# Kernel tuning notes

Hardware: AMD Instinct MI355X
Metric: run time of the kernel (lower is better)

## Reference

```python
import jax, jax.numpy as jnp
import numpy as np

LEAKY = 0.2
K = 8  # hard-coded topk in the torch module
NUM_HEADS = 3


def _knn_mean(x):
    # x: [B, N, C] -> mean of K nearest neighbor features (self included), [B, N, C]
    sq = jnp.sum(x * x, axis=-1)                                   # [B, N]
    d2 = sq[:, :, None] + sq[:, None, :] - 2.0 * jnp.einsum('bnc,bmc->bnm', x, x)
    _, idx = jax.lax.top_k(-d2, K)                                  # smallest distances, [B, N, K]
    neighbors = jax.vmap(lambda xb, ib: xb[ib])(x, idx)             # [B, N, K, C]
    return neighbors.mean(axis=2)


def _mlp(h, W1, b1, W2, b2):
    h = h @ W1.T + b1
    h = jnp.where(h > 0, h, LEAKY * h)                              # LeakyReLU(0.2)
    return h @ W2.T + b2


def _mha(x, Wqkv, bqkv, Wo, bo):
    # x: [S, L, C] self-attention, torch nn.MultiheadAttention semantics
    S, L, C = x.shape
    hd = C // NUM_HEADS
    qkv = x @ Wqkv.T + bqkv                                         # [S, L, 3C]
    q, k, v = jnp.split(qkv, 3, axis=-1)
    def heads(t):
        return t.reshape(S, L, NUM_HEADS, hd).transpose(0, 2, 1, 3)  # [S, H, L, hd]
    q, k, v = heads(q), heads(k), heads(v)
    scores = jnp.einsum('shld,shmd->shlm', q, k) / np.float32(np.sqrt(hd))
    att = jax.nn.softmax(scores, axis=-1)
    o = jnp.einsum('shlm,shmd->shld', att, v).transpose(0, 2, 1, 3).reshape(S, L, C)
    return o @ Wo.T + bo


def setup_inputs() -> dict:
    key = jax.random.key(0)
    ks = jax.random.split(key, 8)
    B, N, C, Hd, HOPS = 4, 4096, 96, 192, 3
    s_in = 1.0 / np.sqrt(C)
    s_hd = 1.0 / np.sqrt(Hd)
    return {
        'xyz': jax.random.normal(ks[0], (B, N, C), jnp.float32),
        'W1': jax.random.normal(ks[1], (HOPS, Hd, C), jnp.float32) * s_in,
        'b1': jnp.zeros((HOPS, Hd), jnp.float32),
        'W2': jax.random.normal(ks[2], (HOPS, C, Hd), jnp.float32) * s_hd,
        'b2': jnp.zeros((HOPS, C), jnp.float32),
        'in_proj_w': jax.random.normal(ks[3], (3 * C, C), jnp.float32) * s_in,
        'in_proj_b': jnp.zeros((3 * C,), jnp.float32),
        'out_proj_w': jax.random.normal(ks[4], (C, C), jnp.float32) * s_in,
        'out_proj_b': jnp.zeros((C,), jnp.float32),
    }


def reference(xyz, W1, b1, W2, b2, in_proj_w, in_proj_b, out_proj_w, out_proj_b):
    B, N, C = xyz.shape
    HOPS = W1.shape[0]
    hop_feats = [xyz]
    cur = xyz
    for h in range(HOPS):
        nb = _knn_mean(cur)                                         # [B, N, C]
        enc = _mlp(nb, W1[h], b1[h], W2[h], b2[h])                  # [B, N, C]
        hop_feats.append(enc)
        cur = enc
    stacked = jnp.stack(hop_feats, axis=2).reshape(B * N, HOPS + 1, C)
    att = _mha(stacked, in_proj_w, in_proj_b, out_proj_w, out_proj_b)
    return att.reshape(B, N, HOPS + 1, C).mean(axis=2)
```

## Files before the change

kernel.cpp:

```cpp
#include <hip/hip_runtime.h>
#include <cfloat>

namespace {

constexpr int Bb    = 4;
constexpr int Nn    = 4096;
constexpr int Cc    = 96;
constexpr int Ll    = 4;
constexpr int NPTS  = Bb * Nn;
constexpr int KP    = 100;
constexpr int CS    = 4;
constexpr int TK    = 10;
constexpr int NCROW = CS * 4 * TK;
constexpr int LP    = 104;
constexpr int NSEL  = 24;

typedef __attribute__((ext_vector_type(8))) short bf16x8;
typedef __attribute__((ext_vector_type(4))) float f32x4;

__device__ inline ushort f2bf(float x) {
    unsigned u = __float_as_uint(x);
    return (ushort)((u + 0x7FFF + ((u >> 16) & 1)) >> 16);
}

template<int T>
__device__ inline void lexins(float v, int vi, float (&bd)[T], int (&bi)[T]) {
    if (v < bd[T - 1] || (v == bd[T - 1] && vi < bi[T - 1])) {
        #pragma unroll
        for (int t = 0; t < T; ++t) {
            if (v < bd[t] || (v == bd[t] && vi < bi[t])) {
                float tv = bd[t]; bd[t] = v;  v  = tv;
                int   ti = bi[t]; bi[t] = vi; vi = ti;
            }
        }
    }
}

template<bool COPY>
__global__ __launch_bounds__(64) void sqcvt_kernel(const float* __restrict__ src0,
                                                   float* __restrict__ A32,
                                                   float* __restrict__ sqnp,
                                                   ushort* __restrict__ A16, int h) {
    const int p = blockIdx.x * 64 + threadIdx.x;
    const float4* xs = reinterpret_cast<const float4*>(
        COPY ? src0 + (size_t)p * Cc : src0 + (size_t)(p * Ll + h) * Cc);
    float4 x[24];
    #pragma unroll
    for (int i = 0; i < 24; ++i) x[i] = xs[i];
    if (COPY) {
        float4* d = reinterpret_cast<float4*>(A32 + (size_t)p * Ll * Cc);
        #pragma unroll
        for (int i = 0; i < 24; ++i) d[i] = x[i];
    }
    float r[8];
    r[0] = __fmul_rn(x[0].x, x[0].x); r[1] = __fmul_rn(x[0].y, x[0].y);
    r[2] = __fmul_rn(x[0].z, x[0].z); r[3] = __fmul_rn(x[0].w, x[0].w);
    r[4] = __fmul_rn(x[1].x, x[1].x); r[5] = __fmul_rn(x[1].y, x[1].y);
    r[6] = __fmul_rn(x[1].z, x[1].z); r[7] = __fmul_rn(x[1].w, x[1].w);
    #pragma unroll
    for (int g = 1; g < 12; ++g) {
        float4 va = x[2 * g], vb = x[2 * g + 1];
        r[0] = __fadd_rn(r[0], __fmul_rn(va.x, va.x));
        r[1] = __fadd_rn(r[1], __fmul_rn(va.y, va.y));
        r[2] = __fadd_rn(r[2], __fmul_rn(va.z, va.z));
        r[3] = __fadd_rn(r[3], __fmul_rn(va.w, va.w));
        r[4] = __fadd_rn(r[4], __fmul_rn(vb.x, vb.x));
        r[5] = __fadd_rn(r[5], __fmul_rn(vb.y, vb.y));
        r[6] = __fadd_rn(r[6], __fmul_rn(vb.z, vb.z));
        r[7] = __fadd_rn(r[7], __fmul_rn(vb.w, vb.w));
    }
    float L = __fadd_rn(__fadd_rn(r[0], r[1]), __fadd_rn(r[2], r[3]));
    float R = __fadd_rn(__fadd_rn(r[4], r[5]), __fadd_rn(r[6], r[7]));
    sqnp[p] = __fadd_rn(L, R);
    #pragma unroll
    for (int j = 0; j < 12; ++j) {
        float4 v0 = x[2 * j], v1 = x[2 * j + 1];
        uint4 o;
        o.x = (unsigned)f2bf(v0.x) | ((unsigned)f2bf(v0.y) << 16);
        o.y = (unsigned)f2bf(v0.z) | ((unsigned)f2bf(v0.w) << 16);
        o.z = (unsigned)f2bf(v1.x) | ((unsigned)f2bf(v1.y) << 16);
        o.w = (unsigned)f2bf(v1.z) | ((unsigned)f2bf(v1.w) << 16);
        *reinterpret_cast<uint4*>(A16 + (size_t)p * 96 + j * 8) = o;
    }
}

__global__ __launch_bounds__(256) void knn_mfma_kernel(const ushort* __restrict__ A16,
                                                       const float* __restrict__ sqnp,
                                                       unsigned* __restrict__ fkey) {
    __shared__ alignas(16) char uqk[20480];
    __shared__ ushort dbt[2][64 * LP];
    __shared__ float  sqf[2][64];
    ushort* qt   = (ushort*)uqk;
    float*  klds = (float*)uqk;

    const int q0    = blockIdx.x * 64;
    const int cs    = blockIdx.y;
    const int pbase = (q0 >> 12) << 12;
    const int col0  = cs * (Nn / CS);
    const int tid   = threadIdx.x;
    const int w     = tid >> 6;
    const int l     = tid & 63;
    constexpr int NCH = (Nn / CS) / 64;

    {
        int r = tid >> 2, q = tid & 3;
        const uint4* s = reinterpret_cast<const uint4*>(A16 + (size_t)(q0 + r) * 96 + q * 24);
        uint4* d = reinterpret_cast<uint4*>(qt + r * LP + q * 24);
        d[0] = s[0]; d[1] = s[1]; d[2] = s[2];
        const uint4* s2 = reinterpret_cast<const uint4*>(
            A16 + (size_t)(pbase + col0 + r) * 96 + q * 24);
        uint4* d2 = reinterpret_cast<uint4*>(dbt[0] + r * LP + q * 24);
        d2[0] = s2[0]; d2[1] = s2[1]; d2[2] = s2[2];
    }
    if (tid < 64) sqf[0][tid] = -0.5f * sqnp[pbase + col0 + tid];
    __syncthreads();

    const int qrow = w * 16 + (l & 15);
    const int koff = (l >> 4) * 8;
    const int lb4  = (l >> 4) * 4;
    bf16x8 bq[3];
    #pragma unroll
    for (int s = 0; s < 3; ++s)
        bq[s] = *reinterpret_cast<const bf16x8*>(qt + qrow * LP + koff + 32 * s);
    __syncthreads();

    unsigned bd[TK];
    #pragma unroll
    for (int t = 0; t < TK; ++t) bd[t] = 0x00800000u;
    float kd = -FLT_MAX;

    for (int c = 0; c < NCH; ++c) {
        const int buf = c & 1;
        if (c + 1 < NCH) {
            int r = tid >> 2, q = tid & 3;
            const uint4* s = reinterpret_cast<const uint4*>(
                A16 + (size_t)(pbase + col0 + (c + 1) * 64 + r) * 96 + q * 24);
            uint4* d = reinterpret_cast<uint4*>(dbt[buf ^ 1] + r * LP + q * 24);
            d[0] = s[0]; d[1] = s[1]; d[2] = s[2];
            if (tid < 64) sqf[buf ^ 1][tid] = -0.5f * sqnp[pbase + col0 + (c + 1) * 64 + tid];
        }

        f32x4 acc[4];
        #pragma unroll
        for (int sub = 0; sub < 4; ++sub) {
            acc[sub] = *reinterpret_cast<const f32x4*>(&sqf[buf][sub * 16 + lb4]);
            #pragma unroll
            for (int s = 0; s < 3; ++s) {
                bf16x8 a = *reinterpret_cast<const bf16x8*>(
                    dbt[buf] + (sub * 16 + (l & 15)) * LP + koff + 32 * s);
                acc[sub] = __builtin_amdgcn_mfma_f32_16x16x32_bf16(a, bq[s], acc[sub], 0, 0, 0);
            }
        }

        unsigned mask = 0;
        #pragma unroll
        for (int sub = 0; sub < 4; ++sub) {
            float m = fmaxf(fmaxf(acc[sub][0], acc[sub][1]),
                            fmaxf(acc[sub][2], acc[sub][3]));
            if (m > kd) {
                *reinterpret_cast<f32x4*>(&klds[tid * 20 + sub * 4]) = acc[sub];
                unsigned mb = (acc[sub][0] > kd ? 1u : 0u) |
                              (acc[sub][1] > kd ? 2u : 0u) |
                              (acc[sub][2] > kd ? 4u : 0u) |
                              (acc[sub][3] > kd ? 8u : 0u);
                mask |= mb << (sub * 4);
            }
        }
        while (mask) {
            int s = __builtin_ctz(mask); mask &= mask - 1;
            float v = klds[tid * 20 + s];
            if (v > kd) {
                unsigned b   = __float_as_uint(v);
                unsigned key = ((b ^ (unsigned)(((int)b >> 31) | 0x80000000)) & ~511u)
                               | (511u - (unsigned)(c * 16 + s));
                #pragma unroll
                for (int t = 0; t < TK; ++t) {
                    unsigned hi = key > bd[t] ? key : bd[t];
                    key         = key > bd[t] ? bd[t] : key;
                    bd[t] = hi;
                }
                unsigned u = bd[TK - 1] & ~511u;
                kd = __uint_as_float((u & 0x80000000u) ? (u ^ 0x80000000u) : ~u);
            }
        }
        __syncthreads();
    }

    const int qg = q0 + qrow;
    const size_t obase = (size_t)qg * NCROW + (cs * 4 + (l >> 4)) * TK;
    #pragma unroll
    for (int t = 0; t < TK; ++t) fkey[obase + t] = bd[t];
}

__device__ inline int decode_idx(unsigned key, int f) {
    int pos = 511 - (int)(key & 511u);
    int c = pos >> 4, s = pos & 15;
    return (f >> 2) * (Nn / CS) + c * 64 + ((s >> 2) << 4) + (f & 3) * 4 + (s & 3);
}

__global__ __launch_bounds__(256) void rescore_mean_kernel(const float* __restrict__ A32,
                                                           const float* __restrict__ sqnp,
                                                           const unsigned* __restrict__ fkey,
                                                           float* __restrict__ nb, int h) {
    __shared__ unsigned kly[32][164];
    __shared__ unsigned m48k[32][48];
    __shared__ unsigned char m48f[32][48];
    __shared__ int      m24[32][NSEL];
    __shared__ float    s24[32][NSEL];
    __shared__ int      sidx[32][8];
    const int tid  = threadIdx.x;
    const int qloc = tid >> 3, sub = tid & 7;
    const int p    = blockIdx.x * 32 + qloc;
    const int base = (p >> 12) << 12;

    {
        const uint4* fs = reinterpret_cast<const uint4*>(fkey + (size_t)p * NCROW + sub * 20);
        #pragma unroll
        for (int m = 0; m < 5; ++m)
            *reinterpret_cast<uint4*>(&kly[qloc][sub * 20 + m * 4]) = fs[m];
    }
    __syncthreads();

    if (sub < 4) {
        unsigned hp = 0;
        #pragma unroll 1
        for (int t = 0; t < 12; ++t) {
            unsigned bk = 0; int bs = 0; bool any = false;
            #pragma unroll
            for (int s = 0; s < 4; ++s) {
                int hs = (hp >> (4 * s)) & 15;
                if (hs < TK) {
                    unsigned k = kly[qloc][(sub * 4 + s) * TK + hs];
                    if (!any || k > bk) { bk = k; bs = s; any = true; }
                }
            }
            m48k[qloc][sub * 12 + t] = bk;
            m48f[qloc][sub * 12 + t] = (unsigned char)(sub * 4 + bs);
            hp += 1u << (4 * bs);
        }
    }
    __syncthreads();

    if (sub == 0) {
        unsigned hp = 0;
        #pragma unroll 1
        for (int t = 0; t < NSEL; ++t) {
            unsigned bk = 0; int bc = 0, bh = 0; bool any = false;
            #pragma unroll
            for (int c = 0; c < 4; ++c) {
                int hs = (hp >> (4 * c)) & 15;
                if (hs < 12) {
                    unsigned k = m48k[qloc][c * 12 + hs];
                    if (!any || k > bk) { bk = k; bc = c; bh = hs; any = true; }
                }
            }
            m24[qloc][t] = decode_idx(bk, (int)m48f[qloc][bc * 12 + bh]);
            hp += 1u << (4 * bc);
        }
    }
    __syncthreads();

    {
        float4 xnr[24];
        const float4* xs = reinterpret_cast<const float4*>(A32 + (size_t)(p * Ll + h) * Cc);
        #pragma unroll
        for (int i = 0; i < 24; ++i) xnr[i] = xs[i];
        const float sqn = sqnp[p];
        #pragma unroll
        for (int c = 0; c < NSEL / 8; ++c) {
            int m = m24[qloc][sub * (NSEL / 8) + c];
            const float4* xm = reinterpret_cast<const float4*>(
                A32 + (size_t)((base + m) * Ll + h) * Cc);
            float l0 = 0.f, l1 = 0.f, l2 = 0.f, l3 = 0.f;
            #pragma unroll
            for (int t = 0; t < 24; ++t) {
                float4 a = xnr[t], b = xm[t];
                l0 = __fadd_rn(l0, __fmul_rn(a.x, b.x));
                l1 = __fadd_rn(l1, __fmul_rn(a.y, b.y));
                l2 = __fadd_rn(l2, __fmul_rn(a.z, b.z));
                l3 = __fadd_rn(l3, __fmul_rn(a.w, b.w));
            }
            float dot = __fadd_rn(__fadd_rn(l0, l1), __fadd_rn(l2, l3));
            s24[qloc][sub * (NSEL / 8) + c] =
                __fsub_rn(__fadd_rn(sqn, sqnp[base + m]), __fmul_rn(2.0f, dot));
        }
    }
    __syncthreads();

    if (sub == 0) {
        float sd[8]; int si[8];
        #pragma unroll
        for (int t = 0; t < 8; ++t) { sd[t] = FLT_MAX; si[t] = 0x7fffffff; }
        #pragma unroll 1
        for (int c = 0; c < NSEL; ++c) lexins<8>(s24[qloc][c], m24[qloc][c], sd, si);
        #pragma unroll
        for (int t = 0; t < 8; ++t) sidx[qloc][t] = si[t];
    }
    __syncthreads();

    {
        float4 rv[8][3];
        #pragma unroll
        for (int k = 0; k < 8; ++k) {
            const float4* rs = reinterpret_cast<const float4*>(
                A32 + (size_t)((base + sidx[qloc][k]) * Ll + h) * Cc + sub * 12);
            rv[k][0] = rs[0]; rv[k][1] = rs[1]; rv[k][2] = rs[2];
        }
        float4* dst = reinterpret_cast<float4*>(nb + (size_t)p * Cc + sub * 12);
        #pragma unroll
        for (int g = 0; g < 3; ++g) {
            float4 o;
            #define NPMEAN(comp) { \
                float L_ = __fadd_rn(__fadd_rn(rv[0][g].comp, rv[1][g].comp), \
                                     __fadd_rn(rv[2][g].comp, rv[3][g].comp)); \
                float R_ = __fadd_rn(__fadd_rn(rv[4][g].comp, rv[5][g].comp), \
                                     __fadd_rn(rv[6][g].comp, rv[7][g].comp)); \
                o.comp = __fmul_rn(__fadd_rn(L_, R_), 0.125f); }
            NPMEAN(x) NPMEAN(y) NPMEAN(z) NPMEAN(w)
            #undef NPMEAN
            dst[g] = o;
        }
    }
}

template<int K, bool LEAKY>
__global__ __launch_bounds__(256) void npgemm_kernel(const float* __restrict__ A,
                                                     const float* __restrict__ W,
                                                     const float* __restrict__ bias,
                                                     float* __restrict__ out,
                                                     int N, int ostride) {
    constexpr int PW = (K == 96) ? 100 : 196;
    __shared__ float w_t[64 * PW];
    const int tx = threadIdx.x, ty = threadIdx.y;
    const int col0 = blockIdx.x * 64;
    const int j = col0 + tx;
    const int i0 = blockIdx.y * 16 + ty * 4;
    {
        int tid = ty * 64 + tx;
        int r = tid >> 2, q = tid & 3;
        constexpr int G = K / 16;
        const int s = r & 7;
        if (col0 + r < N) {
            const float4* src = reinterpret_cast<const float4*>(
                W + (size_t)(col0 + r) * K) + q * G;
            #pragma unroll
            for (int m = 0; m < G; ++m) {
                int g = q * G + m;
                *reinterpret_cast<float4*>(&w_t[r * PW + ((g ^ s) << 2)]) = src[m];
            }
        } else {
            #pragma unroll
            for (int m = 0; m < G; ++m) {
                int g = q * G + m;
                *reinterpret_cast<float4*>(&w_t[r * PW + ((g ^ s) << 2)]) =
                    float4{0.f, 0.f, 0.f, 0.f};
            }
        }
    }
    __syncthreads();
    if (j < N) {
        const float* a0 = A + (size_t)i0 * K;
        const int sx = tx & 7;
        float acc0 = 0.f, acc1 = 0.f, acc2 = 0.f, acc3 = 0.f;
        #pragma unroll
        for (int k4 = 0; k4 < K / 4; ++k4) {
            float4 wv = *reinterpret_cast<const float4*>(&w_t[tx * PW + ((k4 ^ sx) << 2)]);
            float4 a_0 = *reinterpret_cast<const float4*>(a0 + k4 * 4);
            float4 a_1 = *reinterpret_cast<const float4*>(a0 + K + k4 * 4);
            float4 a_2 = *reinterpret_cast<const float4*>(a0 + 2 * K + k4 * 4);
            float4 a_3 = *reinterpret_cast<const float4*>(a0 + 3 * K + k4 * 4);
            acc0 = __builtin_fmaf(a_0.x, wv.x, acc0);
            acc1 = __builtin_fmaf(a_1.x, wv.x, acc1);
            acc2 = __builtin_fmaf(a_2.x, wv.x, acc2);
            acc3 = __builtin_fmaf(a_3.x, wv.x, acc3);
            acc0 = __builtin_fmaf(a_0.y, wv.y, acc0);
            acc1 = __builtin_fmaf(a_1.y, wv.y, acc1);
            acc2 = __builtin_fmaf(a_2.y, wv.y, acc2);
            acc3 = __builtin_fmaf(a_3.y, wv.y, acc3);
            acc0 = __builtin_fmaf(a_0.z, wv.z, acc0);
            acc1 = __builtin_fmaf(a_1.z, wv.z, acc1);
            acc2 = __builtin_fmaf(a_2.z, wv.z, acc2);
            acc3 = __builtin_fmaf(a_3.z, wv.z, acc3);
            acc0 = __builtin_fmaf(a_0.w, wv.w, acc0);
            acc1 = __builtin_fmaf(a_1.w, wv.w, acc1);
            acc2 = __builtin_fmaf(a_2.w, wv.w, acc2);
            acc3 = __builtin_fmaf(a_3.w, wv.w, acc3);
        }
        const float bj = bias[j];
        float v0 = __fadd_rn(acc0, bj), v1 = __fadd_rn(acc1, bj);
        float v2 = __fadd_rn(acc2, bj), v3 = __fadd_rn(acc3, bj);
        if (LEAKY) {
            v0 = v0 > 0.f ? v0 : __fmul_rn(0.2f, v0);
            v1 = v1 > 0.f ? v1 : __fmul_rn(0.2f, v1);
            v2 = v2 > 0.f ? v2 : __fmul_rn(0.2f, v2);
            v3 = v3 > 0.f ? v3 : __fmul_rn(0.2f, v3);
        }
        out[(size_t)i0 * ostride + j] = v0;
        out[(size_t)(i0 + 1) * ostride + j] = v1;
        out[(size_t)(i0 + 2) * ostride + j] = v2;
        out[(size_t)(i0 + 3) * ostride + j] = v3;
    }
}

__device__ inline void stage_row(const float* __restrict__ src, float* __restrict__ tile,
                                 int r, int q) {
    const int s = (r >> 2) & 7;
    #pragma unroll
    for (int m = 0; m < 6; ++m) {
        int g = q * 6 + m;
        float4 v = reinterpret_cast<const float4*>(src)[g];
        *reinterpret_cast<float4*>(&tile[r * KP + ((g ^ s) << 2)]) = v;
    }
}

template<int K>
__global__ __launch_bounds__(256) void gemm_kernel(const float* __restrict__ Ain,
                                                   const float* __restrict__ W,
                                                   const float* __restrict__ bias,
                                                   float* __restrict__ out,
                                                   int Nout, int out_stride) {
    __shared__ float a_t[64 * KP];
    __shared__ float w_t[64 * KP];
    const int row0 = blockIdx.x * 64;
    const int col0 = blockIdx.y * 64;
    const int tid  = threadIdx.x;
    const int tx   = tid & 15;
    const int ty   = tid >> 4;

    float acc[4][4] = {};
    for (int kt = 0; kt < K; kt += 96) {
        __syncthreads();
        {
            int r = tid >> 2, q = tid & 3;
            stage_row(Ain + (size_t)(row0 + r) * K + kt, a_t, r, q);
            if (col0 + r < Nout) {
                stage_row(W + (size_t)(col0 + r) * K + kt, w_t, r, q);
            } else {
                const int s = (r >> 2) & 7;
                #pragma unroll
                for (int m = 0; m < 6; ++m) {
                    int g = q * 6 + m;
                    *reinterpret_cast<float4*>(&w_t[r * KP + ((g ^ s) << 2)]) =
                        float4{0.f, 0.f, 0.f, 0.f};
                }
            }
        }
        __syncthreads();
        const int sa = ty & 7, sb = tx & 7;
        #pragma unroll 4
        for (int k4 = 0; k4 < 24; ++k4) {
            float4 av[4], bv[4];
            const int ga = (k4 ^ sa) << 2, gb = (k4 ^ sb) << 2;
            #pragma unroll
            for (int i = 0; i < 4; ++i)
                av[i] = *reinterpret_cast<const float4*>(&a_t[(ty * 4 + i) * KP + ga]);
            #pragma unroll
            for (int j = 0; j < 4; ++j)
                bv[j] = *reinterpret_cast<const float4*>(&w_t[(tx * 4 + j) * KP + gb]);
            #pragma unroll
            for (int i = 0; i < 4; ++i)
                #pragma unroll
                for (int j = 0; j < 4; ++j)
                    acc[i][j] += av[i].x * bv[j].x + av[i].y * bv[j].y +
                                 av[i].z * bv[j].z + av[i].w * bv[j].w;
        }
    }
    #pragma unroll
    for (int i = 0; i < 4; ++i) {
        int row = row0 + ty * 4 + i;
        #pragma unroll
        for (int j = 0; j < 4; ++j) {
            int col = col0 + tx * 4 + j;
            if (col < Nout)
                out[(size_t)row * out_stride + col] = acc[i][j] + bias[col];
        }
    }
}

__global__ __launch_bounds__(256) void wvo_kernel(const float* __restrict__ ipw,
                                                  const float* __restrict__ ipb,
                                                  const float* __restrict__ opw,
                                                  const float* __restrict__ opb,
                                                  float* __restrict__ wvo,
                                                  float* __restrict__ b2o) {
    int t = blockIdx.x * 256 + threadIdx.x;
    if (t < 96 * 288) {
        int i = t / 288, hj = t - i * 288;
        int hh = hj / 96, j = hj - hh * 96;
        float acc = 0.f;
        #pragma unroll 8
        for (int k = 0; k < 32; ++k)
            acc = __builtin_fmaf(opw[i * 96 + hh * 32 + k],
                                 ipw[(size_t)(192 + hh * 32 + k) * 96 + j], acc);
        wvo[(size_t)i * 288 + hj] = acc;
    }
    if (t < 96) {
        float acc = opb[t];
        #pragma unroll 8
        for (int k = 0; k < 96; ++k)
            acc = __builtin_fmaf(opw[t * 96 + k], ipb[192 + k], acc);
        b2o[t] = acc;
    }
}

__global__ __launch_bounds__(64) void attnmix_kernel(const float* __restrict__ qk,
                                                     const float* __restrict__ A32,
                                                     float* __restrict__ xmixs) {
    int t  = blockIdx.x * 64 + threadIdx.x;
    int p  = t / 3;
    int hh = t - p * 3;
    const float* qb = qk + (size_t)p * 4 * 192 + hh * 32;
    const float* kb = qb + 96;

    float sc[4][4] = {};
    #pragma unroll
    for (int d = 0; d < 32; d += 4) {
        float4 qv[4], kv[4];
        #pragma unroll
        for (int l2 = 0; l2 < 4; ++l2) {
            qv[l2] = *reinterpret_cast<const float4*>(qb + l2 * 192 + d);
            kv[l2] = *reinterpret_cast<const float4*>(kb + l2 * 192 + d);
        }
        #pragma unroll
        for (int l2 = 0; l2 < 4; ++l2)
            #pragma unroll
            for (int m = 0; m < 4; ++m)
                sc[l2][m] += qv[l2].x * kv[m].x + qv[l2].y * kv[m].y +
                             qv[l2].z * kv[m].z + qv[l2].w * kv[m].w;
    }
    const float scale = 0.17677669529663687f;
    float am[4] = {0.f, 0.f, 0.f, 0.f};
    #pragma unroll
    for (int l2 = 0; l2 < 4; ++l2) {
        float s0 = sc[l2][0] * scale, s1 = sc[l2][1] * scale;
        float s2 = sc[l2][2] * scale, s3 = sc[l2][3] * scale;
        float mx = fmaxf(fmaxf(s0, s1), fmaxf(s2, s3));
        float e0 = expf(s0 - mx), e1 = expf(s1 - mx);
        float e2 = expf(s2 - mx), e3 = expf(s3 - mx);
        float inv = 1.f / (e0 + e1 + e2 + e3);
        am[0] += e0 * inv; am[1] += e1 * inv; am[2] += e2 * inv; am[3] += e3 * inv;
    }
    am[0] *= 0.25f; am[1] *= 0.25f; am[2] *= 0.25f; am[3] *= 0.25f;
    const float* xb = A32 + (size_t)p * 4 * 96;
    float* dst = xmixs + (size_t)p * 288 + hh * 96;
    #pragma unroll
    for (int d = 0; d < 96; d += 4) {
        float4 o = {0.f, 0.f, 0.f, 0.f};
        #pragma unroll
        for (int m = 0; m < 4; ++m) {
            float4 v = *reinterpret_cast<const float4*>(xb + m * 96 + d);
            o.x += am[m] * v.x; o.y += am[m] * v.y;
            o.z += am[m] * v.z; o.w += am[m] * v.w;
        }
        *reinterpret_cast<float4*>(dst + d) = o;
    }
}

}

extern "C" void kernel_launch(void* const* d_in, const int* in_sizes, int n_in,
                              void* d_out, int out_size, void* d_ws, size_t ws_size,
                              hipStream_t stream) {
    const float* xyz = (const float*)d_in[0];
    const float* W1  = (const float*)d_in[1];
    const float* b1  = (const float*)d_in[2];
    const float* W2  = (const float*)d_in[3];
    const float* b2  = (const float*)d_in[4];
    const float* ipw = (const float*)d_in[5];
    const float* ipb = (const float*)d_in[6];
    const float* opw = (const float*)d_in[7];
    const float* opb = (const float*)d_in[8];

    char* ws = (char*)d_ws;
    float*    A32  = (float*)ws;
    float*    sqnp = (float*)(ws + 25165824);
    unsigned* fkey = (unsigned*)(ws + 25231360);
    float*    nb   = (float*)(ws + 35717120);
    float*    h1   = (float*)(ws + 42008576);
    ushort*   A16  = (ushort*)(ws + 54591488);
    float*    qkc4  = (float*)(ws + 25231360);
    float*    xmixs = (float*)(ws + 75563008);
    float*    wvo   = (float*)(ws + 94437376);
    float*    b2o   = (float*)(ws + 94547968);

    for (int h = 0; h < 3; ++h) {
        if (h == 0)
            sqcvt_kernel<true><<<256, 64, 0, stream>>>(xyz, A32, sqnp, A16, 0);
        else
            sqcvt_kernel<false><<<256, 64, 0, stream>>>(A32, A32, sqnp, A16, h);
        knn_mfma_kernel<<<dim3(NPTS / 64, CS), 256, 0, stream>>>(A16, sqnp, fkey);
        rescore_mean_kernel<<<NPTS / 32, 256, 0, stream>>>(A32, sqnp, fkey, nb, h);
        npgemm_kernel<96, true><<<dim3(3, NPTS / 16), dim3(64, 4), 0, stream>>>(
            nb, W1 + (size_t)h * 192 * 96, b1 + h * 192, h1, 192, 192);
        npgemm_kernel<192, false><<<dim3(2, NPTS / 16), dim3(64, 4), 0, stream>>>(
            h1, W2 + (size_t)h * 96 * 192, b2 + h * 96, A32 + (h + 1) * 96, 96, Ll * Cc);
    }

    wvo_kernel<<<108, 256, 0, stream>>>(ipw, ipb, opw, opb, wvo, b2o);
    gemm_kernel<96><<<dim3(65536 / 64, 3), 256, 0, stream>>>(
        A32, ipw, ipb, qkc4, 192, 192);
    attnmix_kernel<<<NPTS * 3 / 64, 64, 0, stream>>>(qkc4, A32, xmixs);
    gemm_kernel<288><<<dim3(NPTS / 64, 2), 256, 0, stream>>>(
        xmixs, wvo, b2o, (float*)d_out, 96, 96);
}
```

Before: 762.8 us.

## Shrink LDS in kNN and MLP GEMM kernels to raise occupancy

The kNN MFMA kernel drops its double-buffered LDS tile. It prefetches the next chunk into registers and writes it to a single LDS buffer after a barrier, which adds a second __syncthreads per chunk. The npgemm kernel now tiles the K dimension in 96-wide slices, so the K=192 variant uses a 100-float-stride LDS tile instead of a 196 one. Both changes cut shared memory per block to allow more resident blocks. The cost is extra synchronization and serialized load/compute in the kNN loop.

```diff
diff --git a/kernel.cpp b/kernel.cpp
--- a/kernel.cpp
+++ b/kernel.cpp
@@ -88,8 +88,8 @@
                                                        const float* __restrict__ sqnp,
                                                        unsigned* __restrict__ fkey) {
     __shared__ alignas(16) char uqk[20480];
-    __shared__ ushort dbt[2][64 * LP];
-    __shared__ float  sqf[2][64];
+    __shared__ ushort dbt[64 * LP];
+    __shared__ float  sqf[64];
     ushort* qt   = (ushort*)uqk;
     float*  klds = (float*)uqk;
 
@@ -101,18 +101,18 @@
     const int w     = tid >> 6;
     const int l     = tid & 63;
     constexpr int NCH = (Nn / CS) / 64;
+    const int r4 = tid >> 2, q4 = tid & 3;
 
     {
-        int r = tid >> 2, q = tid & 3;
-        const uint4* s = reinterpret_cast<const uint4*>(A16 + (size_t)(q0 + r) * 96 + q * 24);
-        uint4* d = reinterpret_cast<uint4*>(qt + r * LP + q * 24);
+        const uint4* s = reinterpret_cast<const uint4*>(A16 + (size_t)(q0 + r4) * 96 + q4 * 24);
+        uint4* d = reinterpret_cast<uint4*>(qt + r4 * LP + q4 * 24);
         d[0] = s[0]; d[1] = s[1]; d[2] = s[2];
         const uint4* s2 = reinterpret_cast<const uint4*>(
-            A16 + (size_t)(pbase + col0 + r) * 96 + q * 24);
-        uint4* d2 = reinterpret_cast<uint4*>(dbt[0] + r * LP + q * 24);
+            A16 + (size_t)(pbase + col0 + r4) * 96 + q4 * 24);
+        uint4* d2 = reinterpret_cast<uint4*>(dbt + r4 * LP + q4 * 24);
         d2[0] = s2[0]; d2[1] = s2[1]; d2[2] = s2[2];
     }
-    if (tid < 64) sqf[0][tid] = -0.5f * sqnp[pbase + col0 + tid];
+    if (tid < 64) sqf[tid] = -0.5f * sqnp[pbase + col0 + tid];
     __syncthreads();
 
     const int qrow = w * 16 + (l & 15);
@@ -130,24 +130,23 @@
     float kd = -FLT_MAX;
 
     for (int c = 0; c < NCH; ++c) {
-        const int buf = c & 1;
-        if (c + 1 < NCH) {
-            int r = tid >> 2, q = tid & 3;
+        uint4 pf0, pf1, pf2; float sqpf = 0.f;
+        const bool hasNext = (c + 1 < NCH);
+        if (hasNext) {
             const uint4* s = reinterpret_cast<const uint4*>(
-                A16 + (size_t)(pbase + col0 + (c + 1) * 64 + r) * 96 + q * 24);
-            uint4* d = reinterpret_cast<uint4*>(dbt[buf ^ 1] + r * LP + q * 24);
-            d[0] = s[0]; d[1] = s[1]; d[2] = s[2];
-            if (tid < 64) sqf[buf ^ 1][tid] = -0.5f * sqnp[pbase + col0 + (c + 1) * 64 + tid];
+                A16 + (size_t)(pbase + col0 + (c + 1) * 64 + r4) * 96 + q4 * 24);
+            pf0 = s[0]; pf1 = s[1]; pf2 = s[2];
+            if (tid < 64) sqpf = sqnp[pbase + col0 + (c + 1) * 64 + tid];
         }
 
         f32x4 acc[4];
         #pragma unroll
         for (int sub = 0; sub < 4; ++sub) {
-            acc[sub] = *reinterpret_cast<const f32x4*>(&sqf[buf][sub * 16 + lb4]);
+            acc[sub] = *reinterpret_cast<const f32x4*>(&sqf[sub * 16 + lb4]);
             #pragma unroll
             for (int s = 0; s < 3; ++s) {
                 bf16x8 a = *reinterpret_cast<const bf16x8*>(
-                    dbt[buf] + (sub * 16 + (l & 15)) * LP + koff + 32 * s);
+                    dbt + (sub * 16 + (l & 15)) * LP + koff + 32 * s);
                 acc[sub] = __builtin_amdgcn_mfma_f32_16x16x32_bf16(a, bq[s], acc[sub], 0, 0, 0);
             }
         }
@@ -184,6 +183,12 @@
             }
         }
         __syncthreads();
+        if (hasNext) {
+            uint4* d = reinterpret_cast<uint4*>(dbt + r4 * LP + q4 * 24);
+            d[0] = pf0; d[1] = pf1; d[2] = pf2;
+            if (tid < 64) sqf[tid] = -0.5f * sqpf;
+        }
+        __syncthreads();
     }
 
     const int qg = q0 + qrow;
@@ -329,63 +334,67 @@
                                                      const float* __restrict__ bias,
                                                      float* __restrict__ out,
                                                      int N, int ostride) {
-    constexpr int PW = (K == 96) ? 100 : 196;
+    constexpr int PW = 100;
     __shared__ float w_t[64 * PW];
     const int tx = threadIdx.x, ty = threadIdx.y;
     const int col0 = blockIdx.x * 64;
     const int j = col0 + tx;
     const int i0 = blockIdx.y * 16 + ty * 4;
-    {
-        int tid = ty * 64 + tx;
-        int r = tid >> 2, q = tid & 3;
-        constexpr int G = K / 16;
-        const int s = r & 7;
+    const int tid = ty * 64 + tx;
+    const int r = tid >> 2, q = tid & 3;
+    const int sw = r & 7;
+    const int sx = tx & 7;
+    const float* a0 = A + (size_t)i0 * K;
+    float acc0 = 0.f, acc1 = 0.f, acc2 = 0.f, acc3 = 0.f;
+
+    for (int kt = 0; kt < K; kt += 96) {
+        __syncthreads();
         if (col0 + r < N) {
             const float4* src = reinterpret_cast<const float4*>(
-                W + (size_t)(col0 + r) * K) + q * G;
-            #pragma unroll
-            for (int m = 0; m < G; ++m) {
-                int g = q * G + m;
-                *reinterpret_cast<float4*>(&w_t[r * PW + ((g ^ s) << 2)]) = src[m];
+                W + (size_t)(col0 + r) * K + kt) + q * 6;
+            #pragma unroll
+            for (int m = 0; m < 6; ++m) {
+                int g = q * 6 + m;
+                *reinterpret_cast<float4*>(&w_t[r * PW + ((g ^ sw) << 2)]) = src[m];
             }
         } else {
             #pragma unroll
-            for (int m = 0; m < G; ++m) {
-                int g = q * G + m;
-                *reinterpret_cast<float4*>(&w_t[r * PW + ((g ^ s) << 2)]) =
+            for (int m = 0; m < 6; ++m) {
+                int g = q * 6 + m;
+                *reinterpret_cast<float4*>(&w_t[r * PW + ((g ^ sw) << 2)]) =
                     float4{0.f, 0.f, 0.f, 0.f};
             }
         }
-    }
-    __syncthreads();
+        __syncthreads();
+        if (j < N) {
+            #pragma unroll
+            for (int k4 = 0; k4 < 24; ++k4) {
+                float4 wv = *reinterpret_cast<const float4*>(
+                    &w_t[tx * PW + ((k4 ^ sx) << 2)]);
+                float4 a_0 = *reinterpret_cast<const float4*>(a0 + kt + k4 * 4);
+                float4 a_1 = *reinterpret_cast<const float4*>(a0 + K + kt + k4 * 4);
+                float4 a_2 = *reinterpret_cast<const float4*>(a0 + 2 * K + kt + k4 * 4);
+                float4 a_3 = *reinterpret_cast<const float4*>(a0 + 3 * K + kt + k4 * 4);
+                acc0 = __builtin_fmaf(a_0.x, wv.x, acc0);
+                acc1 = __builtin_fmaf(a_1.x, wv.x, acc1);
+                acc2 = __builtin_fmaf(a_2.x, wv.x, acc2);
+                acc3 = __builtin_fmaf(a_3.x, wv.x, acc3);
+                acc0 = __builtin_fmaf(a_0.y, wv.y, acc0);
+                acc1 = __builtin_fmaf(a_1.y, wv.y, acc1);
+                acc2 = __builtin_fmaf(a_2.y, wv.y, acc2);
+                acc3 = __builtin_fmaf(a_3.y, wv.y, acc3);
+                acc0 = __builtin_fmaf(a_0.z, wv.z, acc0);
+                acc1 = __builtin_fmaf(a_1.z, wv.z, acc1);
+                acc2 = __builtin_fmaf(a_2.z, wv.z, acc2);
+                acc3 = __builtin_fmaf(a_3.z, wv.z, acc3);
+                acc0 = __builtin_fmaf(a_0.w, wv.w, acc0);
+                acc1 = __builtin_fmaf(a_1.w, wv.w, acc1);
+                acc2 = __builtin_fmaf(a_2.w, wv.w, acc2);
+                acc3 = __builtin_fmaf(a_3.w, wv.w, acc3);
+            }
+        }
+    }
     if (j < N) {
-        const float* a0 = A + (size_t)i0 * K;
-        const int sx = tx & 7;
-        float acc0 = 0.f, acc1 = 0.f, acc2 = 0.f, acc3 = 0.f;
-        #pragma unroll
-        for (int k4 = 0; k4 < K / 4; ++k4) {
-            float4 wv = *reinterpret_cast<const float4*>(&w_t[tx * PW + ((k4 ^ sx) << 2)]);
-            float4 a_0 = *reinterpret_cast<const float4*>(a0 + k4 * 4);
-            float4 a_1 = *reinterpret_cast<const float4*>(a0 + K + k4 * 4);
-            float4 a_2 = *reinterpret_cast<const float4*>(a0 + 2 * K + k4 * 4);
-            float4 a_3 = *reinterpret_cast<const float4*>(a0 + 3 * K + k4 * 4);
-            acc0 = __builtin_fmaf(a_0.x, wv.x, acc0);
-            acc1 = __builtin_fmaf(a_1.x, wv.x, acc1);
-            acc2 = __builtin_fmaf(a_2.x, wv.x, acc2);
-            acc3 = __builtin_fmaf(a_3.x, wv.x, acc3);
-            acc0 = __builtin_fmaf(a_0.y, wv.y, acc0);
-            acc1 = __builtin_fmaf(a_1.y, wv.y, acc1);
-            acc2 = __builtin_fmaf(a_2.y, wv.y, acc2);
-            acc3 = __builtin_fmaf(a_3.y, wv.y, acc3);
-            acc0 = __builtin_fmaf(a_0.z, wv.z, acc0);
-            acc1 = __builtin_fmaf(a_1.z, wv.z, acc1);
-            acc2 = __builtin_fmaf(a_2.z, wv.z, acc2);
-            acc3 = __builtin_fmaf(a_3.z, wv.z, acc3);
-            acc0 = __builtin_fmaf(a_0.w, wv.w, acc0);
-            acc1 = __builtin_fmaf(a_1.w, wv.w, acc1);
-            acc2 = __builtin_fmaf(a_2.w, wv.w, acc2);
-            acc3 = __builtin_fmaf(a_3.w, wv.w, acc3);
-        }
         const float bj = bias[j];
         float v0 = __fadd_rn(acc0, bj), v1 = __fadd_rn(acc1, bj);
         float v2 = __fadd_rn(acc2, bj), v3 = __fadd_rn(acc3, bj);
```

Result: faster. 728.9 us (-4.4%).
